# Performance work log

Measured on AMD Instinct MI355X. Metric: run time of the kernel, lower is better.

Reference implementation:

```python
import jax, jax.numpy as jnp
import numpy as np

N_NODES = 100000
N_EDGES = 1600000
D_IN = 128
D_HID = 128
N_CLASSES = 4
N_GRAPHS = 512


def setup_inputs() -> dict:
    key = jax.random.key(0)
    ks = jax.random.split(key, 10)
    x = jax.random.normal(ks[0], (N_NODES, D_IN), dtype=jnp.float32)
    edge_index = jax.random.randint(ks[1], (2, N_EDGES), 0, N_NODES, dtype=jnp.int64)
    batch = jnp.sort(jax.random.randint(ks[2], (N_NODES,), 0, N_GRAPHS, dtype=jnp.int64))
    s = 1.0 / np.sqrt(D_IN)
    W1l = jax.random.uniform(ks[3], (D_HID, D_IN), jnp.float32, -s, s)
    W1r = jax.random.uniform(ks[4], (D_HID, D_IN), jnp.float32, -s, s)
    b1 = jnp.zeros((D_HID,), jnp.float32)
    s2 = 1.0 / np.sqrt(D_HID)
    W2l = jax.random.uniform(ks[5], (D_HID, D_HID), jnp.float32, -s2, s2)
    W2r = jax.random.uniform(ks[6], (D_HID, D_HID), jnp.float32, -s2, s2)
    b2 = jnp.zeros((D_HID,), jnp.float32)
    Wlin = jax.random.uniform(ks[7], (N_CLASSES, D_HID), jnp.float32, -s2, s2)
    blin = jax.random.uniform(ks[8], (N_CLASSES,), jnp.float32, -s2, s2)
    return {"x": x, "edge_index": edge_index, "batch": batch,
            "W1l": W1l, "b1": b1, "W1r": W1r,
            "W2l": W2l, "b2": b2, "W2r": W2r,
            "Wlin": Wlin, "blin": blin}


def _sage_conv(x, src, dst, deg_inv, W_l, b, W_r):
    # mean-aggregate neighbor features (messages flow src -> dst)
    agg = jax.ops.segment_sum(x[src], dst, num_segments=N_NODES) * deg_inv
    return agg @ W_l.T + b + x @ W_r.T


def reference(x, edge_index, batch, W1l, b1, W1r, W2l, b2, W2r, Wlin, blin):
    src, dst = edge_index[0], edge_index[1]
    ones = jnp.ones((src.shape[0],), x.dtype)
    deg = jax.ops.segment_sum(ones, dst, num_segments=N_NODES)
    deg_inv = (1.0 / jnp.maximum(deg, 1.0))[:, None]

    h = jax.nn.relu(_sage_conv(x, src, dst, deg_inv, W1l, b1, W1r))
    h = jax.nn.relu(_sage_conv(h, src, dst, deg_inv, W2l, b2, W2r))

    # global mean pool over graphs
    gsum = jax.ops.segment_sum(h, batch, num_segments=N_GRAPHS)
    gcnt = jax.ops.segment_sum(jnp.ones((N_NODES,), h.dtype), batch, num_segments=N_GRAPHS)
    pooled = gsum / jnp.maximum(gcnt, 1.0)[:, None]

    # dropout is identity in eval mode
    return pooled @ Wlin.T + blin
```

## Files before the change

kernel.cpp:

```cpp
#include <hip/hip_runtime.h>
#include <hip/hip_bf16.h>


#define NN 100000
#define NE 1600000
#define DH 128
#define NG 512
#define CSTRIDE 48
#define NPREP 6250

#define SUBSH 8
#define SUBN  256
#define NSUB  391
#define CAP   4608
#define NSCAN 256
#define ESPS  6250
#define GBLK  2048

#define PSUM_SCALE  1048576.0f
#define PSUM_INV    (1.0f/1048576.0f)

typedef __hip_bfloat16 bf16;
typedef __bf16 bf16x8 __attribute__((ext_vector_type(8)));
typedef float  f32x4  __attribute__((ext_vector_type(4)));
typedef float  f32x2  __attribute__((ext_vector_type(2)));
typedef unsigned u32x2 __attribute__((ext_vector_type(2)));
typedef unsigned u32x4 __attribute__((ext_vector_type(4)));
typedef unsigned char u8;

__device__ __forceinline__ void bf8_to_f(uint4 q, float* w) {
    union { unsigned u; float f; } t;
    t.u = q.x << 16;          w[0] = t.f;
    t.u = q.x & 0xffff0000u;  w[1] = t.f;
    t.u = q.y << 16;          w[2] = t.f;
    t.u = q.y & 0xffff0000u;  w[3] = t.f;
    t.u = q.z << 16;          w[4] = t.f;
    t.u = q.z & 0xffff0000u;  w[5] = t.f;
    t.u = q.w << 16;          w[6] = t.f;
    t.u = q.w & 0xffff0000u;  w[7] = t.f;
}

__device__ __forceinline__ unsigned pack4_fp8(float a, float b, float c, float d) {
    int p = __builtin_amdgcn_cvt_pk_fp8_f32(a, b, 0, false);
    p = __builtin_amdgcn_cvt_pk_fp8_f32(c, d, p, true);
    return (unsigned)p;
}


__global__ __launch_bounds__(256) void k_prep(
    const int* __restrict__ ei, int* __restrict__ ccnt,
    const float* __restrict__ x, u8* __restrict__ fq,
    const float* __restrict__ w0, const float* __restrict__ w1,
    const float* __restrict__ w2, const float* __restrict__ w3,
    bf16* __restrict__ wb,
    const int* __restrict__ batch, int* __restrict__ cnt)
{
    const int bid = blockIdx.x, tid = threadIdx.x;

    if (bid < NSCAN) {
        __shared__ int c[NSUB];
        for (int i = tid; i < NSUB; i += 256) c[i] = 0;
        __syncthreads();
        const int e0 = bid * ESPS;
        for (int e = e0 + tid; e < e0 + ESPS; e += 256) {
            int d = __builtin_nontemporal_load(ei + NE + e);
            atomicAdd(&c[d >> SUBSH], 1);
        }
        __syncthreads();
        for (int i = tid; i < NSUB; i += 256) ccnt[i * NSCAN + bid] = c[i];
        return;
    }

    const int pb = bid - NSCAN;
    {
        int g = pb * 256 + tid;
        const f32x4* s = (const f32x4*)(x + (size_t)g * 8);
        f32x4 u0 = __builtin_nontemporal_load(s);
        f32x4 u1 = __builtin_nontemporal_load(s + 1);
        u32x2 v;
        v[0] = pack4_fp8(u0[0], u0[1], u0[2], u0[3]);
        v[1] = pack4_fp8(u1[0], u1[1], u1[2], u1[3]);
        __builtin_nontemporal_store(v, (u32x2*)(fq + (size_t)g * 8));
    }
    if (pb < 256) {
        int gid = pb * 256 + tid;
        int m = gid >> 14, i = gid & 16383;
        const float* src = (m == 0) ? w0 : (m == 1) ? w1 : (m == 2) ? w2 : w3;
        wb[gid] = __float2bfloat16(src[i]);
    } else if (pb < 258) {
        int g = (pb - 256) * 256 + tid;
        if (g < NG) {
            int lo0 = 0, hi0 = NN, lo1 = 0, hi1 = NN;
            while (lo0 < hi0) { int m = (lo0 + hi0) >> 1; if (batch[m] < g)     lo0 = m + 1; else hi0 = m; }
            while (lo1 < hi1) { int m = (lo1 + hi1) >> 1; if (batch[m] < g + 1) lo1 = m + 1; else hi1 = m; }
            cnt[g] = lo1 - lo0;
        }
    } else if (pb == 258) {
        if (tid < 8) {
            uint4 z = {0u, 0u, 0u, 0u};
            ((uint4*)(fq + (size_t)NN * DH))[tid] = z;
        }
    }
}


__global__ __launch_bounds__(256) void k_rowscan(
    const int* __restrict__ ccnt, int* __restrict__ bofs, int* __restrict__ tot)
{
    const int g = blockIdx.x, t = threadIdx.x;
    __shared__ int s[256];
    int v = ccnt[g * NSCAN + t];
    s[t] = v;
    __syncthreads();
    #pragma unroll
    for (int off = 1; off < 256; off <<= 1) {
        int tmp = (t >= off) ? s[t - off] : 0;
        __syncthreads();
        s[t] += tmp;
        __syncthreads();
    }
    bofs[g * NSCAN + t] = s[t] - v;
    if (t == 255) tot[g] = s[255];
}


__global__ __launch_bounds__(256) void k_scatter(
    const int* __restrict__ ei, const int* __restrict__ bofs,
    unsigned* __restrict__ pe)
{
    const int s = blockIdx.x, tid = threadIdx.x;
    __shared__ int rank[NSUB];
    for (int g = tid; g < NSUB; g += 256)
        rank[g] = g * CAP + bofs[g * NSCAN + s];
    __syncthreads();

    const int e0 = s * ESPS;
    for (int e = e0 + tid; e < e0 + ESPS; e += 256) {
        int d   = __builtin_nontemporal_load(ei + NE + e);
        int src = __builtin_nontemporal_load(ei + e);
        int g = d >> SUBSH;
        int pos = atomicAdd(&rank[g], 1);
        if (pos < (g + 1) * CAP)
            pe[pos] = ((unsigned)(d & (SUBN - 1)) << 17) | (unsigned)src;
    }
}


__global__ __launch_bounds__(256) void k_fill2(
    const unsigned* __restrict__ pe, const int* __restrict__ tot,
    int* __restrict__ deg, int* __restrict__ col)
{
    const int g = blockIdx.x, tid = threadIdx.x;
    __shared__ int degL[SUBN];
    degL[tid] = 0;
    __syncthreads();

    const int lo = g * CAP;
    const int n  = min(tot[g], CAP);
    const int nb = g << SUBSH;
    for (int e = lo + tid; e < lo + n; e += 256) {
        unsigned p = pe[e];
        int src = (int)(p & 0x1FFFFu);
        int dl  = (int)(p >> 17);
        int pos = atomicAdd(&degL[dl], 1);
        if (pos < CSTRIDE) col[(nb + dl) * CSTRIDE + pos] = src;
    }
    __syncthreads();

    int node = nb + tid;
    if (node < NN) deg[node] = degL[tid];
}


__global__ __launch_bounds__(256) void k_gather(
    const int* __restrict__ deg, const int* __restrict__ col,
    const u8* __restrict__ fq, bf16* __restrict__ agg)
{
    const int lane = threadIdx.x & 63;
    const int qsub = lane >> 4;
    const int l4   = lane & 15;
    const unsigned l8 = (unsigned)l4 * 8u;
    const int wid  = blockIdx.x * 4 + (threadIdx.x >> 6);
    const int NSTR = GBLK * 4 * 2;

    int nA = wid * 2;

    int dgrA = deg[nA];
    int dgrB = deg[nA + 1];
    int vrawA = (lane < CSTRIDE) ? col[nA * CSTRIDE + lane] : 0;
    int vrawB = (lane < CSTRIDE) ? col[(nA + 1) * CSTRIDE + lane] : 0;

    while (true) {
        const int nN = nA + NSTR;
        const bool more = nN < NN;
        int dgrAN = 0, dgrBN = 0, vrawAN = 0, vrawBN = 0;
        if (more) {
            dgrAN = deg[nN];
            dgrBN = deg[nN + 1];
            vrawAN = (lane < CSTRIDE) ? col[nN * CSTRIDE + lane] : 0;
            vrawBN = (lane < CSTRIDE) ? col[(nN + 1) * CSTRIDE + lane] : 0;
        }

        const int dgsA = __builtin_amdgcn_readfirstlane(dgrA);
        const int dgsB = __builtin_amdgcn_readfirstlane(dgrB);
        const int dgA = dgsA > CSTRIDE ? CSTRIDE : dgsA;
        const int dgB = dgsB > CSTRIDE ? CSTRIDE : dgsB;
        const int dgM = dgA > dgB ? dgA : dgB;
        int vidxA = (lane < dgA) ? vrawA : NN;
        int vidxB = (lane < dgB) ? vrawB : NN;

        f32x2 aA0 = {0.f, 0.f}, aA1 = {0.f, 0.f}, aA2 = {0.f, 0.f}, aA3 = {0.f, 0.f};
        f32x2 aB0 = {0.f, 0.f}, aB1 = {0.f, 0.f}, aB2 = {0.f, 0.f}, aB3 = {0.f, 0.f};

        for (int e = 0; e < dgM; e += 16) {
            int sA0 = __shfl(vidxA, e + qsub,      64);
            int sA1 = __shfl(vidxA, e + 4 + qsub,  64);
            int sA2 = __shfl(vidxA, e + 8 + qsub,  64);
            int sA3 = __shfl(vidxA, e + 12 + qsub, 64);
            int sB0 = __shfl(vidxB, e + qsub,      64);
            int sB1 = __shfl(vidxB, e + 4 + qsub,  64);
            int sB2 = __shfl(vidxB, e + 8 + qsub,  64);
            int sB3 = __shfl(vidxB, e + 12 + qsub, 64);
            uint2 qA0 = *(const uint2*)(fq + (((unsigned)sA0 << 7) + l8));
            uint2 qA1 = *(const uint2*)(fq + (((unsigned)sA1 << 7) + l8));
            uint2 qA2 = *(const uint2*)(fq + (((unsigned)sA2 << 7) + l8));
            uint2 qA3 = *(const uint2*)(fq + (((unsigned)sA3 << 7) + l8));
            uint2 qB0 = *(const uint2*)(fq + (((unsigned)sB0 << 7) + l8));
            uint2 qB1 = *(const uint2*)(fq + (((unsigned)sB1 << 7) + l8));
            uint2 qB2 = *(const uint2*)(fq + (((unsigned)sB2 << 7) + l8));
            uint2 qB3 = *(const uint2*)(fq + (((unsigned)sB3 << 7) + l8));
            aA0 += __builtin_amdgcn_cvt_pk_f32_fp8((int)qA0.x, false);
            aA1 += __builtin_amdgcn_cvt_pk_f32_fp8((int)qA0.x, true);
            aA2 += __builtin_amdgcn_cvt_pk_f32_fp8((int)qA0.y, false);
            aA3 += __builtin_amdgcn_cvt_pk_f32_fp8((int)qA0.y, true);
            aA0 += __builtin_amdgcn_cvt_pk_f32_fp8((int)qA1.x, false);
            aA1 += __builtin_amdgcn_cvt_pk_f32_fp8((int)qA1.x, true);
            aA2 += __builtin_amdgcn_cvt_pk_f32_fp8((int)qA1.y, false);
            aA3 += __builtin_amdgcn_cvt_pk_f32_fp8((int)qA1.y, true);
            aA0 += __builtin_amdgcn_cvt_pk_f32_fp8((int)qA2.x, false);
            aA1 += __builtin_amdgcn_cvt_pk_f32_fp8((int)qA2.x, true);
            aA2 += __builtin_amdgcn_cvt_pk_f32_fp8((int)qA2.y, false);
            aA3 += __builtin_amdgcn_cvt_pk_f32_fp8((int)qA2.y, true);
            aA0 += __builtin_amdgcn_cvt_pk_f32_fp8((int)qA3.x, false);
            aA1 += __builtin_amdgcn_cvt_pk_f32_fp8((int)qA3.x, true);
            aA2 += __builtin_amdgcn_cvt_pk_f32_fp8((int)qA3.y, false);
            aA3 += __builtin_amdgcn_cvt_pk_f32_fp8((int)qA3.y, true);
            aB0 += __builtin_amdgcn_cvt_pk_f32_fp8((int)qB0.x, false);
            aB1 += __builtin_amdgcn_cvt_pk_f32_fp8((int)qB0.x, true);
            aB2 += __builtin_amdgcn_cvt_pk_f32_fp8((int)qB0.y, false);
            aB3 += __builtin_amdgcn_cvt_pk_f32_fp8((int)qB0.y, true);
            aB0 += __builtin_amdgcn_cvt_pk_f32_fp8((int)qB1.x, false);
            aB1 += __builtin_amdgcn_cvt_pk_f32_fp8((int)qB1.x, true);
            aB2 += __builtin_amdgcn_cvt_pk_f32_fp8((int)qB1.y, false);
            aB3 += __builtin_amdgcn_cvt_pk_f32_fp8((int)qB1.y, true);
            aB0 += __builtin_amdgcn_cvt_pk_f32_fp8((int)qB2.x, false);
            aB1 += __builtin_amdgcn_cvt_pk_f32_fp8((int)qB2.x, true);
            aB2 += __builtin_amdgcn_cvt_pk_f32_fp8((int)qB2.y, false);
            aB3 += __builtin_amdgcn_cvt_pk_f32_fp8((int)qB2.y, true);
            aB0 += __builtin_amdgcn_cvt_pk_f32_fp8((int)qB3.x, false);
            aB1 += __builtin_amdgcn_cvt_pk_f32_fp8((int)qB3.x, true);
            aB2 += __builtin_amdgcn_cvt_pk_f32_fp8((int)qB3.y, false);
            aB3 += __builtin_amdgcn_cvt_pk_f32_fp8((int)qB3.y, true);
        }

        float rA[8] = {aA0[0], aA0[1], aA1[0], aA1[1], aA2[0], aA2[1], aA3[0], aA3[1]};
        float rB[8] = {aB0[0], aB0[1], aB1[0], aB1[1], aB2[0], aB2[1], aB3[0], aB3[1]};
        #pragma unroll
        for (int i = 0; i < 8; ++i) {
            rA[i] += __shfl_xor(rA[i], 16, 64);
            rB[i] += __shfl_xor(rB[i], 16, 64);
            rA[i] += __shfl_xor(rA[i], 32, 64);
            rB[i] += __shfl_xor(rB[i], 32, 64);
        }

        if (qsub == 0) {
            float di = 1.0f / fmaxf((float)dgsA, 1.0f);
            union { bf16 b[8]; u32x4 u; } pk;
            #pragma unroll
            for (int i = 0; i < 8; ++i) pk.b[i] = __float2bfloat16(rA[i] * di);
            __builtin_nontemporal_store(pk.u, (u32x4*)(agg + nA * DH + l4 * 8));
        } else if (qsub == 1) {
            float di = 1.0f / fmaxf((float)dgsB, 1.0f);
            union { bf16 b[8]; u32x4 u; } pk;
            #pragma unroll
            for (int i = 0; i < 8; ++i) pk.b[i] = __float2bfloat16(rB[i] * di);
            __builtin_nontemporal_store(pk.u, (u32x4*)(agg + (nA + 1) * DH + l4 * 8));
        }

        if (!more) break;
        nA = nN;
        dgrA = dgrAN; dgrB = dgrBN; vrawA = vrawAN; vrawB = vrawBN;
    }
}


#define WSTR 136

template <bool POOL>
__global__ __launch_bounds__(256, 4) void k_layer(
    const bf16* __restrict__ agg, const u8* __restrict__ xq,
    const bf16* __restrict__ Wlb, const bf16* __restrict__ Wrb,
    const float* __restrict__ bias,
    u8* __restrict__ outq, int* __restrict__ psum,
    const int* __restrict__ batch)
{
    __shared__ bf16 wl[128 * WSTR];
    __shared__ int  bb[128];

    const int tid  = threadIdx.x;
    const int wave = tid >> 6;
    const int lane = tid & 63;
    const int lm   = lane & 15;
    const int kg   = lane >> 4;
    const int base = blockIdx.x * 128;
    const int wbase = base + wave * 32;

    const int r0 = min(wbase + lm,      NN - 1);
    const int r1 = min(wbase + 16 + lm, NN - 1);

    if (POOL && tid < 128) bb[tid] = batch[min(base + tid, NN - 1)];

    {
        const int row = tid >> 1, half = tid & 1;
        const uint4* src = (const uint4*)(Wlb + row * DH + half * 64);
        uint4* dst = (uint4*)(wl + row * WSTR + half * 64);
        #pragma unroll
        for (int i = 0; i < 8; ++i) dst[i] = src[i];
    }
    __syncthreads();

    f32x4 acc[2][8];
    #pragma unroll
    for (int i = 0; i < 2; ++i)
        #pragma unroll
        for (int t = 0; t < 8; ++t)
            acc[i][t] = (f32x4){0.f, 0.f, 0.f, 0.f};

    #pragma unroll
    for (int kc = 0; kc < 4; ++kc) {
        const int ko = kc * 32 + kg * 8;
        bf16x8 a0 = *(const bf16x8*)(agg + r0 * DH + ko);
        bf16x8 a1 = *(const bf16x8*)(agg + r1 * DH + ko);
        #pragma unroll
        for (int t = 0; t < 8; ++t) {
            bf16x8 b = *(const bf16x8*)(wl + (t * 16 + lm) * WSTR + ko);
            acc[0][t] = __builtin_amdgcn_mfma_f32_16x16x32_bf16(a0, b, acc[0][t], 0, 0, 0);
            acc[1][t] = __builtin_amdgcn_mfma_f32_16x16x32_bf16(a1, b, acc[1][t], 0, 0, 0);
        }
    }
    __syncthreads();

    {
        const int row = tid >> 1, half = tid & 1;
        const uint4* src = (const uint4*)(Wrb + row * DH + half * 64);
        uint4* dst = (uint4*)(wl + row * WSTR + half * 64);
        #pragma unroll
        for (int i = 0; i < 8; ++i) dst[i] = src[i];
    }
    __syncthreads();

    #pragma unroll
    for (int kc = 0; kc < 4; ++kc) {
        const int ko = kc * 32 + kg * 8;
        bf16x8 a0, a1;
        uint2 q0 = *(const uint2*)(xq + (size_t)r0 * DH + ko);
        uint2 q1 = *(const uint2*)(xq + (size_t)r1 * DH + ko);
        f32x2 c0 = __builtin_amdgcn_cvt_pk_f32_fp8((int)q0.x, false);
        f32x2 c1 = __builtin_amdgcn_cvt_pk_f32_fp8((int)q0.x, true);
        f32x2 c2 = __builtin_amdgcn_cvt_pk_f32_fp8((int)q0.y, false);
        f32x2 c3 = __builtin_amdgcn_cvt_pk_f32_fp8((int)q0.y, true);
        a0[0] = (__bf16)c0[0]; a0[1] = (__bf16)c0[1];
        a0[2] = (__bf16)c1[0]; a0[3] = (__bf16)c1[1];
        a0[4] = (__bf16)c2[0]; a0[5] = (__bf16)c2[1];
        a0[6] = (__bf16)c3[0]; a0[7] = (__bf16)c3[1];
        c0 = __builtin_amdgcn_cvt_pk_f32_fp8((int)q1.x, false);
        c1 = __builtin_amdgcn_cvt_pk_f32_fp8((int)q1.x, true);
        c2 = __builtin_amdgcn_cvt_pk_f32_fp8((int)q1.y, false);
        c3 = __builtin_amdgcn_cvt_pk_f32_fp8((int)q1.y, true);
        a1[0] = (__bf16)c0[0]; a1[1] = (__bf16)c0[1];
        a1[2] = (__bf16)c1[0]; a1[3] = (__bf16)c1[1];
        a1[4] = (__bf16)c2[0]; a1[5] = (__bf16)c2[1];
        a1[6] = (__bf16)c3[0]; a1[7] = (__bf16)c3[1];
        #pragma unroll
        for (int t = 0; t < 8; ++t) {
            bf16x8 b = *(const bf16x8*)(wl + (t * 16 + lm) * WSTR + ko);
            acc[0][t] = __builtin_amdgcn_mfma_f32_16x16x32_bf16(a0, b, acc[0][t], 0, 0, 0);
            acc[1][t] = __builtin_amdgcn_mfma_f32_16x16x32_bf16(a1, b, acc[1][t], 0, 0, 0);
        }
    }
    __syncthreads();

    bf16* ob = wl;
    const int quad = lane >> 4;
    #pragma unroll
    for (int i = 0; i < 2; ++i) {
        #pragma unroll
        for (int r = 0; r < 4; ++r) {
            const int lr = wave * 32 + i * 16 + quad * 4 + r;
            const int n  = base + lr;
            #pragma unroll
            for (int t = 0; t < 8; ++t) {
                const int f = t * 16 + lm;
                float v = fmaxf(acc[i][t][r] + bias[f], 0.f);
                if (POOL && n >= NN) v = 0.f;
                ob[lr * DH + f] = __float2bfloat16(v);
            }
        }
    }
    __syncthreads();

    if (!POOL) {
        uint2* d = (uint2*)(outq + (size_t)base * DH);
        #pragma unroll
        for (int i = 0; i < 8; ++i) {
            const int idx = i * 256 + tid;
            const int n = base + (idx >> 4);
            if (n < NN) {
                uint4 s = ((const uint4*)ob)[idx];
                float w[8];
                bf8_to_f(s, w);
                uint2 o;
                o.x = pack4_fp8(w[0], w[1], w[2], w[3]);
                o.y = pack4_fp8(w[4], w[5], w[6], w[7]);
                d[idx] = o;
            }
        }
    } else {
        const int f = tid & 127, h = tid >> 7;
        float rs = 0.f;
        int cur = bb[h * 64];
        #pragma unroll 8
        for (int r = 0; r < 64; ++r) {
            const int row = h * 64 + r;
            float v = __bfloat162float(ob[row * DH + f]);
            int b = bb[row];
            if (b != cur) {
                atomicAdd(&psum[cur * DH + f], __float2int_rn(rs * PSUM_SCALE));
                rs = 0.f; cur = b;
            }
            rs += v;
        }
        atomicAdd(&psum[cur * DH + f], __float2int_rn(rs * PSUM_SCALE));
    }
}


__global__ __launch_bounds__(256) void k_final(
    const int* __restrict__ psum, const int* __restrict__ cnt,
    const float* __restrict__ Wlin, const float* __restrict__ blin,
    float* __restrict__ out)
{
    int gid = blockIdx.x * 256 + threadIdx.x;
    if (gid >= NG * 4) return;
    int gph = gid >> 2, c = gid & 3;
    const int* p = psum + gph * DH;
    const float* w = Wlin + c * DH;
    float s = 0.f;
    #pragma unroll 8
    for (int k = 0; k < DH; ++k)
        s += (float)p[k] * w[k];
    float inv = 1.0f / fmaxf((float)cnt[gph], 1.0f);
    out[gid] = s * PSUM_INV * inv + blin[c];
}

extern "C" void kernel_launch(void* const* d_in, const int* in_sizes, int n_in,
                              void* d_out, int out_size, void* d_ws, size_t ws_size,
                              hipStream_t stream) {
    const float* x     = (const float*)d_in[0];
    const int*   ei    = (const int*)d_in[1];
    const int*   batch = (const int*)d_in[2];
    const float* W1l   = (const float*)d_in[3];
    const float* b1    = (const float*)d_in[4];
    const float* W1r   = (const float*)d_in[5];
    const float* W2l   = (const float*)d_in[6];
    const float* b2    = (const float*)d_in[7];
    const float* W2r   = (const float*)d_in[8];
    const float* Wlin  = (const float*)d_in[9];
    const float* blin  = (const float*)d_in[10];
    float* out = (float*)d_out;

    char* base = (char*)d_ws;
    int*      deg  = (int*)(base + 64);
    int*      cnt  = (int*)(base + 400064);
    int*      psum = (int*)(base + 402112);
    bf16*     wb   = (bf16*)(base + 664256);
    int*      ccnt = (int*)(base + 795328);
    int*      bofs = (int*)(base + 1195712);
    int*      tot  = (int*)(base + 1596096);
    int*      col  = (int*)(base + 1597696);
    bf16*     agg  = (bf16*)(base + 20797696);
    u8*       fq   = (u8*)(base + 46397696);
    unsigned* pe   = (unsigned*)(base + 59200000);

    bf16* W1lb = wb;
    bf16* W1rb = wb + 16384;
    bf16* W2lb = wb + 32768;
    bf16* W2rb = wb + 49152;

    hipMemsetAsync(base + 402112, 0, 262144, stream);

    k_prep<<<NSCAN + NPREP, 256, 0, stream>>>(
        ei, ccnt, x, fq, W1l, W1r, W2l, W2r, wb, batch, cnt);
    k_rowscan<<<NSUB, 256, 0, stream>>>(ccnt, bofs, tot);
    k_scatter<<<NSCAN, 256, 0, stream>>>(ei, bofs, pe);
    k_fill2<<<NSUB, 256, 0, stream>>>(pe, tot, deg, col);

    k_gather<<<GBLK, 256, 0, stream>>>(deg, col, fq, agg);
    k_layer<false><<<(NN + 127) / 128, 256, 0, stream>>>(agg, fq, W1lb, W1rb, b1,
                                                         fq, nullptr, nullptr);

    k_gather<<<GBLK, 256, 0, stream>>>(deg, col, fq, agg);
    k_layer<true><<<(NN + 127) / 128, 256, 0, stream>>>(agg, fq, W2lb, W2rb, b2,
                                                        nullptr, psum, batch);

    k_final<<<8, 256, 0, stream>>>(psum, cnt, Wlin, blin, out);
}
```

Before: 288.8 us.

## Fuse CSR fill into gather using shared-memory adjacency per 128-node bucket

The separate fill kernel that wrote per-node degree and a padded column array to global memory is removed. Each gather block now takes a 128-node bucket, builds the adjacency lists in LDS from the bucketed edge stream, and immediately runs the mean aggregation. The bucket size is halved and the capacity adjusted to match. This removes the global col/deg write and reread and one launch, but the LDS fill is now repeated for both layers, and 782 blocks of 512 threads with about 25KB LDS each may lower occupancy and latency hiding compared with the old persistent, prefetching gather.

```diff
diff --git a/kernel.cpp b/kernel.cpp
--- a/kernel.cpp
+++ b/kernel.cpp
@@ -9,13 +9,12 @@
 #define CSTRIDE 48
 #define NPREP 6250
 
-#define SUBSH 8
-#define SUBN  256
-#define NSUB  391
-#define CAP   4608
+#define SUBSH 7
+#define SUBN  128
+#define NSUB  782
+#define CAP   2432
 #define NSCAN 256
 #define ESPS  6250
-#define GBLK  2048
 
 #define PSUM_SCALE  1048576.0f
 #define PSUM_INV    (1.0f/1048576.0f)
@@ -146,68 +145,49 @@
 }
 
 
-__global__ __launch_bounds__(256) void k_fill2(
+__global__ __launch_bounds__(512) void k_fillgather(
     const unsigned* __restrict__ pe, const int* __restrict__ tot,
-    int* __restrict__ deg, int* __restrict__ col)
-{
+    const u8* __restrict__ fq, bf16* __restrict__ agg)
+{
+    __shared__ int colL[SUBN][CSTRIDE];
+    __shared__ int degL[SUBN];
+
     const int g = blockIdx.x, tid = threadIdx.x;
-    __shared__ int degL[SUBN];
-    degL[tid] = 0;
+    if (tid < SUBN) degL[tid] = 0;
     __syncthreads();
 
     const int lo = g * CAP;
     const int n  = min(tot[g], CAP);
-    const int nb = g << SUBSH;
-    for (int e = lo + tid; e < lo + n; e += 256) {
+    for (int e = lo + tid; e < lo + n; e += 512) {
         unsigned p = pe[e];
         int src = (int)(p & 0x1FFFFu);
         int dl  = (int)(p >> 17);
         int pos = atomicAdd(&degL[dl], 1);
-        if (pos < CSTRIDE) col[(nb + dl) * CSTRIDE + pos] = src;
-    }
-    __syncthreads();
-
-    int node = nb + tid;
-    if (node < NN) deg[node] = degL[tid];
-}
-
-
-__global__ __launch_bounds__(256) void k_gather(
-    const int* __restrict__ deg, const int* __restrict__ col,
-    const u8* __restrict__ fq, bf16* __restrict__ agg)
-{
-    const int lane = threadIdx.x & 63;
+        if (pos < CSTRIDE) colL[dl][pos] = src;
+    }
+    __syncthreads();
+
+    const int lane = tid & 63;
+    const int wave = tid >> 6;
     const int qsub = lane >> 4;
     const int l4   = lane & 15;
     const unsigned l8 = (unsigned)l4 * 8u;
-    const int wid  = blockIdx.x * 4 + (threadIdx.x >> 6);
-    const int NSTR = GBLK * 4 * 2;
-
-    int nA = wid * 2;
-
-    int dgrA = deg[nA];
-    int dgrB = deg[nA + 1];
-    int vrawA = (lane < CSTRIDE) ? col[nA * CSTRIDE + lane] : 0;
-    int vrawB = (lane < CSTRIDE) ? col[(nA + 1) * CSTRIDE + lane] : 0;
-
-    while (true) {
-        const int nN = nA + NSTR;
-        const bool more = nN < NN;
-        int dgrAN = 0, dgrBN = 0, vrawAN = 0, vrawBN = 0;
-        if (more) {
-            dgrAN = deg[nN];
-            dgrBN = deg[nN + 1];
-            vrawAN = (lane < CSTRIDE) ? col[nN * CSTRIDE + lane] : 0;
-            vrawBN = (lane < CSTRIDE) ? col[(nN + 1) * CSTRIDE + lane] : 0;
-        }
-
+    const int nb = g << SUBSH;
+
+    #pragma unroll 1
+    for (int i = 0; i < 8; ++i) {
+        const int ln = wave * 16 + i * 2;
+        const int nA = nb + ln;
+
+        int dgrA = degL[ln];
+        int dgrB = degL[ln + 1];
         const int dgsA = __builtin_amdgcn_readfirstlane(dgrA);
         const int dgsB = __builtin_amdgcn_readfirstlane(dgrB);
         const int dgA = dgsA > CSTRIDE ? CSTRIDE : dgsA;
         const int dgB = dgsB > CSTRIDE ? CSTRIDE : dgsB;
         const int dgM = dgA > dgB ? dgA : dgB;
-        int vidxA = (lane < dgA) ? vrawA : NN;
-        int vidxB = (lane < dgB) ? vrawB : NN;
+        int vidxA = (lane < dgA) ? colL[ln][lane] : NN;
+        int vidxB = (lane < dgB) ? colL[ln + 1][lane] : NN;
 
         f32x2 aA0 = {0.f, 0.f}, aA1 = {0.f, 0.f}, aA2 = {0.f, 0.f}, aA3 = {0.f, 0.f};
         f32x2 aB0 = {0.f, 0.f}, aB1 = {0.f, 0.f}, aB2 = {0.f, 0.f}, aB3 = {0.f, 0.f};
@@ -266,30 +246,30 @@
         float rA[8] = {aA0[0], aA0[1], aA1[0], aA1[1], aA2[0], aA2[1], aA3[0], aA3[1]};
         float rB[8] = {aB0[0], aB0[1], aB1[0], aB1[1], aB2[0], aB2[1], aB3[0], aB3[1]};
         #pragma unroll
-        for (int i = 0; i < 8; ++i) {
-            rA[i] += __shfl_xor(rA[i], 16, 64);
-            rB[i] += __shfl_xor(rB[i], 16, 64);
-            rA[i] += __shfl_xor(rA[i], 32, 64);
-            rB[i] += __shfl_xor(rB[i], 32, 64);
+        for (int k = 0; k < 8; ++k) {
+            rA[k] += __shfl_xor(rA[k], 16, 64);
+            rB[k] += __shfl_xor(rB[k], 16, 64);
+            rA[k] += __shfl_xor(rA[k], 32, 64);
+            rB[k] += __shfl_xor(rB[k], 32, 64);
         }
 
         if (qsub == 0) {
-            float di = 1.0f / fmaxf((float)dgsA, 1.0f);
-            union { bf16 b[8]; u32x4 u; } pk;
-            #pragma unroll
-            for (int i = 0; i < 8; ++i) pk.b[i] = __float2bfloat16(rA[i] * di);
-            __builtin_nontemporal_store(pk.u, (u32x4*)(agg + nA * DH + l4 * 8));
+            if (nA < NN) {
+                float di = 1.0f / fmaxf((float)dgsA, 1.0f);
+                union { bf16 b[8]; u32x4 u; } pk;
+                #pragma unroll
+                for (int k = 0; k < 8; ++k) pk.b[k] = __float2bfloat16(rA[k] * di);
+                __builtin_nontemporal_store(pk.u, (u32x4*)(agg + nA * DH + l4 * 8));
+            }
         } else if (qsub == 1) {
-            float di = 1.0f / fmaxf((float)dgsB, 1.0f);
-            union { bf16 b[8]; u32x4 u; } pk;
-            #pragma unroll
-            for (int i = 0; i < 8; ++i) pk.b[i] = __float2bfloat16(rB[i] * di);
-            __builtin_nontemporal_store(pk.u, (u32x4*)(agg + (nA + 1) * DH + l4 * 8));
-        }
-
-        if (!more) break;
-        nA = nN;
-        dgrA = dgrAN; dgrB = dgrBN; vrawA = vrawAN; vrawB = vrawBN;
+            if (nA + 1 < NN) {
+                float di = 1.0f / fmaxf((float)dgsB, 1.0f);
+                union { bf16 b[8]; u32x4 u; } pk;
+                #pragma unroll
+                for (int k = 0; k < 8; ++k) pk.b[k] = __float2bfloat16(rB[k] * di);
+                __builtin_nontemporal_store(pk.u, (u32x4*)(agg + (nA + 1) * DH + l4 * 8));
+            }
+        }
     }
 }
 
@@ -480,36 +460,33 @@
     float* out = (float*)d_out;
 
     char* base = (char*)d_ws;
-    int*      deg  = (int*)(base + 64);
-    int*      cnt  = (int*)(base + 400064);
-    int*      psum = (int*)(base + 402112);
-    bf16*     wb   = (bf16*)(base + 664256);
-    int*      ccnt = (int*)(base + 795328);
-    int*      bofs = (int*)(base + 1195712);
-    int*      tot  = (int*)(base + 1596096);
-    int*      col  = (int*)(base + 1597696);
-    bf16*     agg  = (bf16*)(base + 20797696);
-    u8*       fq   = (u8*)(base + 46397696);
-    unsigned* pe   = (unsigned*)(base + 59200000);
+    int*      cnt  = (int*)(base + 64);
+    int*      psum = (int*)(base + 2112);
+    bf16*     wb   = (bf16*)(base + 264256);
+    int*      ccnt = (int*)(base + 395328);
+    int*      bofs = (int*)(base + 1196096);
+    int*      tot  = (int*)(base + 1996864);
+    bf16*     agg  = (bf16*)(base + 2000064);
+    u8*       fq   = (u8*)(base + 27600064);
+    unsigned* pe   = (unsigned*)(base + 40400192);
 
     bf16* W1lb = wb;
     bf16* W1rb = wb + 16384;
     bf16* W2lb = wb + 32768;
     bf16* W2rb = wb + 49152;
 
-    hipMemsetAsync(base + 402112, 0, 262144, stream);
+    hipMemsetAsync(base + 2112, 0, 262144, stream);
 
     k_prep<<<NSCAN + NPREP, 256, 0, stream>>>(
         ei, ccnt, x, fq, W1l, W1r, W2l, W2r, wb, batch, cnt);
     k_rowscan<<<NSUB, 256, 0, stream>>>(ccnt, bofs, tot);
     k_scatter<<<NSCAN, 256, 0, stream>>>(ei, bofs, pe);
-    k_fill2<<<NSUB, 256, 0, stream>>>(pe, tot, deg, col);
-
-    k_gather<<<GBLK, 256, 0, stream>>>(deg, col, fq, agg);
+
+    k_fillgather<<<NSUB, 512, 0, stream>>>(pe, tot, fq, agg);
     k_layer<false><<<(NN + 127) / 128, 256, 0, stream>>>(agg, fq, W1lb, W1rb, b1,
                                                          fq, nullptr, nullptr);
 
-    k_gather<<<GBLK, 256, 0, stream>>>(deg, col, fq, agg);
+    k_fillgather<<<NSUB, 512, 0, stream>>>(pe, tot, fq, agg);
     k_layer<true><<<(NN + 127) / 128, 256, 0, stream>>>(agg, fq, W2lb, W2rb, b2,
                                                         nullptr, psum, batch);
 
```

After: 328.4 us. 1.14x slower.
